# Optimization experiments

Hardware: AMD Instinct MI355X
Metric: run time of the kernel (lower is better)

## Reference

```python
import jax, jax.numpy as jnp
import numpy as np

B, S, D, H = 4, 2048, 1024, 16


def setup_inputs() -> dict:
    key = jax.random.key(0)
    ks = jax.random.split(key, 6)
    scale = 0.02
    return {
        "x": jax.random.normal(ks[0], (B, S, D), dtype=jnp.float32),
        "Wq": jax.random.normal(ks[1], (D, D), dtype=jnp.float32) * scale,
        "bq": jnp.zeros((D,), dtype=jnp.float32),
        "Wk": jax.random.normal(ks[2], (D, D), dtype=jnp.float32) * scale,
        "Wv": jax.random.normal(ks[3], (D, D), dtype=jnp.float32) * scale,
        "bv": jnp.zeros((D,), dtype=jnp.float32),
        "Wc": jax.random.normal(ks[4], (D, D), dtype=jnp.float32) * scale,
        "bc": jnp.zeros((D,), dtype=jnp.float32),
        "n_head": H,
    }


def reference(x, Wq, bq, Wk, Wv, bv, Wc, bc, n_head):
    # Projections (Conv1D == linear; k_proj has no bias since key_bias=False)
    q = x @ Wq + bq                      # [B, S, d_attn]
    k = x @ Wk                           # [B, S, d_attn]
    v = x @ Wv + bv                      # [B, S, d_attn]

    b, s, d_attn = q.shape
    d_head = d_attn // n_head
    # split heads -> [B, H, S, d_head]
    qh = q.reshape(b, s, n_head, d_head).transpose(0, 2, 1, 3)
    kh = k.reshape(b, s, n_head, d_head).transpose(0, 2, 1, 3)
    vh = v.reshape(b, s, n_head, d_head).transpose(0, 2, 1, 3)

    # scale applied to both q and k: 1/sqrt(sqrt(d_head))
    softmax_scale = 1.0 / np.sqrt(np.sqrt(d_head))
    qh = qh * softmax_scale
    kh = kh * softmax_scale

    w = jnp.einsum("bhqd,bhkd->bhqk", qh, kh)
    wtype = w.dtype
    w = w.astype(jnp.float32)
    n_q, n_k = w.shape[-2], w.shape[-1]
    # tril mask with diagonal offset n_k - n_q (supports incremental decode)
    mask = jnp.tril(jnp.ones((n_q, n_k), dtype=jnp.float32), k=n_k - n_q)[None, None]
    NEG = -1000000000.0
    w = w * mask + NEG * (1.0 - mask)
    w = jax.nn.softmax(w, axis=-1).astype(wtype)
    # attn_dropout rate 0 -> identity

    a = jnp.einsum("bhqk,bhkd->bhqd", w, vh)
    a = a.transpose(0, 2, 1, 3).reshape(b, s, d_attn)  # merge heads
    a = a @ Wc + bc
    # resid_dropout rate 0 -> identity
    hidden_state = jnp.stack([k, v])  # [2, B, S, d_attn]
    return (a, hidden_state)
```

## Files before the change

kernel.cpp:

```cpp
#include <hip/hip_runtime.h>
#include <stdint.h>

#define B_ 4
#define S_ 2048
#define D_ 1024
#define H_ 16
#define DH_ 64
#define MROWS (B_*S_)

typedef unsigned short ushortT;
typedef __attribute__((ext_vector_type(8))) short bf16x8;
typedef __attribute__((ext_vector_type(4))) float f32x4;

#define FLAG_BF16 1u
#define FLAG_F32  2u

__device__ __forceinline__ float b2f(ushortT u) {
  union { unsigned int i; float f; } v; v.i = ((unsigned int)u) << 16; return v.f;
}
__device__ __forceinline__ ushortT f2b(float f) {
  union { float f; unsigned int i; } v; v.f = f;
  unsigned int r = v.i + 0x7fffu + ((v.i >> 16) & 1u);
  return (ushortT)(r >> 16);
}

__device__ __forceinline__ float loadf(const ushortT* p) { return b2f(*p); }
__device__ __forceinline__ float loadf(const float* p)   { return *p; }
__device__ __forceinline__ unsigned int tob(ushortT u) { return u; }
__device__ __forceinline__ unsigned int tob(float f)   { return f2b(f); }

__device__ __forceinline__ void load8b(const ushortT* p, ushortT* u) {
  *(uint4*)u = *(const uint4*)p;
}
__device__ __forceinline__ void load8b(const float* p, ushortT* u) {
  float4 a = ((const float4*)p)[0], b = ((const float4*)p)[1];
  u[0] = f2b(a.x); u[1] = f2b(a.y); u[2] = f2b(a.z); u[3] = f2b(a.w);
  u[4] = f2b(b.x); u[5] = f2b(b.y); u[6] = f2b(b.z); u[7] = f2b(b.w);
}
template <typename T>
__device__ __forceinline__ void load16b(const T* p, ushortT* u) {
  load8b(p, u); load8b(p + 8, u + 8);
}

__device__ __forceinline__ void storef(ushortT* p, float v) { *p = f2b(v); }
__device__ __forceinline__ void storef(float* p, float v)   { *p = v; }

__device__ __forceinline__ void gload16(const ushortT* g, ushortT* l) {
  __builtin_amdgcn_global_load_lds(
      (const __attribute__((address_space(1))) void*)g,
      (__attribute__((address_space(3))) void*)l, 16, 0, 0);
}

__global__ void detect_dtype(const unsigned int* __restrict__ xw,
                             unsigned int* __restrict__ flag) {
  int lane = threadIdx.x;
  int cnt = 0;
  for (int i = lane; i < 2048; i += 64) {
    unsigned int e = (xw[i] >> 7) & 0xFFu;
    cnt += (e >= 0x68u && e <= 0x8Au) ? 1 : 0;
  }
#pragma unroll
  for (int off = 32; off; off >>= 1) cnt += __shfl_down(cnt, off);
  if (lane == 0) *flag = (cnt > 1024) ? FLAG_BF16 : FLAG_F32;
}

__global__ __launch_bounds__(256) void cvt_x_f32(
    const float* __restrict__ x, ushortT* __restrict__ xb,
    const unsigned int* __restrict__ flag) {
  if (*flag != FLAG_F32) return;
  const int total = MROWS * D_ / 8;
  for (int i = blockIdx.x * 256 + threadIdx.x; i < total; i += gridDim.x * 256) {
    float4 a = ((const float4*)x)[2 * i], b = ((const float4*)x)[2 * i + 1];
    ushortT u[8];
    u[0] = f2b(a.x); u[1] = f2b(a.y); u[2] = f2b(a.z); u[3] = f2b(a.w);
    u[4] = f2b(b.x); u[5] = f2b(b.y); u[6] = f2b(b.z); u[7] = f2b(b.w);
    ((uint4*)xb)[i] = *(uint4*)u;
  }
}

#define BK 32
#define BSTRIDE 40
#define GEMM_LDS (128 * BK + 128 * BSTRIDE)

template <typename TB, typename TOUT>
__device__ __forceinline__ void gemm_body(
    const ushortT* __restrict__ A, const TB* __restrict__ Bm,
    const TB* __restrict__ bias, TOUT* __restrict__ C, ushortT* smem)
{
  const int K = 1024, N = 1024;
  ushortT* As = smem;
  ushortT* Bs = smem + 128 * BK;
  int m0 = blockIdx.x * 128;
  int n0 = blockIdx.y * 128;
  int t = threadIdx.x;
  int lane = t & 63;
  int w = t >> 6;
  int wm = w >> 1, wn = w & 1;

  f32x4 acc[4][4] = {};

  const ushortT* a_src0 = A + (size_t)(m0 + (t >> 2)) * K + (t & 3) * 8;
  const ushortT* a_src1 = a_src0 + (size_t)64 * K;
  ushortT* a_dst0 = &As[(16 * w) * BK];
  ushortT* a_dst1 = &As[(64 + 16 * w) * BK];

  int cB = t & 127, r0 = (t >> 7) * 16;
  const TB* Bp0 = Bm + (size_t)r0 * N + n0 + cB;

  TB breg[16];
#pragma unroll
  for (int j = 0; j < 16; ++j) breg[j] = Bp0[(size_t)j * N];

  for (int kt = 0; kt < K; kt += BK) {
    gload16(a_src0 + kt, a_dst0);
    gload16(a_src1 + kt, a_dst1);
    {
      unsigned int* bd = (unsigned int*)&Bs[cB * BSTRIDE + r0];
#pragma unroll
      for (int j = 0; j < 8; ++j) {
        unsigned int lo = tob(breg[2 * j]);
        unsigned int hi = tob(breg[2 * j + 1]);
        bd[j] = lo | (hi << 16);
      }
    }
    __syncthreads();

    if (kt + BK < K) {
      const TB* bp = Bp0 + (size_t)(kt + BK) * N;
#pragma unroll
      for (int j = 0; j < 16; ++j) breg[j] = bp[(size_t)j * N];
    }

    int kq = (lane >> 4) * 8;
    int lm = lane & 15;
    bf16x8 af[4], bf[4];
#pragma unroll
    for (int mi = 0; mi < 4; ++mi)
      af[mi] = *(const bf16x8*)&As[(wm * 64 + mi * 16 + lm) * BK + kq];
#pragma unroll
    for (int ni = 0; ni < 4; ++ni)
      bf[ni] = *(const bf16x8*)&Bs[(wn * 64 + ni * 16 + lm) * BSTRIDE + kq];
#pragma unroll
    for (int mi = 0; mi < 4; ++mi)
#pragma unroll
      for (int ni = 0; ni < 4; ++ni)
        acc[mi][ni] = __builtin_amdgcn_mfma_f32_16x16x32_bf16(af[mi], bf[ni], acc[mi][ni], 0, 0, 0);
    __syncthreads();
  }

#pragma unroll
  for (int ni = 0; ni < 4; ++ni) {
    int col = n0 + wn * 64 + ni * 16 + (lane & 15);
    float bvv = bias ? loadf(bias + col) : 0.f;
#pragma unroll
    for (int mi = 0; mi < 4; ++mi) {
      int rbase = m0 + wm * 64 + mi * 16 + ((lane >> 4) * 4);
#pragma unroll
      for (int r = 0; r < 4; ++r)
        storef(C + (size_t)(rbase + r) * N + col, acc[mi][ni][r] + bvv);
    }
  }
}

#define KSTR 72
#define ATTN_LDS (2 * 64 * KSTR + 8 * 16 * KSTR)

template <typename TKV>
__device__ __forceinline__ void attn_body(
    const ushortT* __restrict__ Q, const TKV* __restrict__ Kh,
    const TKV* __restrict__ Vh, ushortT* __restrict__ O, ushortT* smem,
    int x, int h, int b)
{
  ushortT* Ks = smem;
  ushortT* Vs = smem + 64 * KSTR;
  ushortT* Ps = smem + 2 * 64 * KSTR;

  const int t = threadIdx.x, w = t >> 6, lane = t & 63;
  const int l15 = lane & 15, quad = lane >> 4;

  bf16x8 onesf;
  {
    ushortT u[8];
#pragma unroll
    for (int j = 0; j < 8; ++j) u[j] = 0x3F80;
    onesf = *(bf16x8*)u;
  }

  const TKV* kb = Kh + (size_t)(b * S_) * D_ + h * DH_;
  const TKV* vb = Vh + (size_t)(b * S_) * D_ + h * DH_;
  ushortT* Pw = Ps + w * (16 * KSTR);

  const int krow = t >> 3, kc = t & 7;
  const int vk = lane;

  for (int pi = 0; pi < 2; ++pi) {
    const int qt = pi ? (15 - x) : x;
    const int q0 = qt * 128;

    bf16x8 qf[2];
    {
      const ushortT* qp = Q + ((size_t)(b * S_) + q0 + w * 16 + l15) * D_ + h * DH_ + quad * 8;
#pragma unroll
      for (int c = 0; c < 2; ++c) {
        ushortT u[8];
        load8b(qp + c * 32, u);
        qf[c] = *(bf16x8*)u;
      }
    }

    f32x4 oac[4];
#pragma unroll
    for (int ni = 0; ni < 4; ++ni) oac[ni] = (f32x4){0.f, 0.f, 0.f, 0.f};
    f32x4 lac = (f32x4){0.f, 0.f, 0.f, 0.f};

    ushortT kr[8], vr[8];
    const int t0max = q0 + 64;

    {
      const TKV* kp = kb + (size_t)krow * D_ + kc * 8;
      load8b(kp, kr);
      const TKV* vp = vb + (size_t)vk * D_ + w * 8;
      load8b(vp, vr);
    }

    for (int t0 = 0; t0 <= t0max; t0 += 64) {
      *(uint4*)&Ks[krow * KSTR + kc * 8] = *(uint4*)kr;
#pragma unroll
      for (int j = 0; j < 8; ++j) Vs[(w * 8 + j) * KSTR + vk] = vr[j];
      __syncthreads();

      if (t0 + 64 <= t0max) {
        const TKV* kp = kb + (size_t)(t0 + 64 + krow) * D_ + kc * 8;
        load8b(kp, kr);
        const TKV* vp = vb + (size_t)(t0 + 64 + vk) * D_ + w * 8;
        load8b(vp, vr);
      }

      f32x4 sac[4];
#pragma unroll
      for (int ni = 0; ni < 4; ++ni) sac[ni] = (f32x4){0.f, 0.f, 0.f, 0.f};
      __builtin_amdgcn_s_setprio(1);
#pragma unroll
      for (int c = 0; c < 2; ++c)
#pragma unroll
        for (int ni = 0; ni < 4; ++ni) {
          bf16x8 bk = *(const bf16x8*)&Ks[(16 * ni + l15) * KSTR + c * 32 + quad * 8];
          sac[ni] = __builtin_amdgcn_mfma_f32_16x16x32_bf16(qf[c], bk, sac[ni], 0, 0, 0);
        }
      __builtin_amdgcn_s_setprio(0);

      if (t0 >= q0) {
        int koff = t0 - q0;
        int rowloc = w * 16 + quad * 4;
#pragma unroll
        for (int ni = 0; ni < 4; ++ni) {
          int kcol = koff + 16 * ni + l15;
#pragma unroll
          for (int r = 0; r < 4; ++r)
            if (kcol > rowloc + r) sac[ni][r] = -1e30f;
        }
      }

#pragma unroll
      for (int ni = 0; ni < 4; ++ni)
#pragma unroll
        for (int r = 0; r < 4; ++r) {
          float p = __expf(sac[ni][r] * 0.125f);
          Pw[(quad * 4 + r) * KSTR + 16 * ni + l15] = f2b(p);
        }

      __builtin_amdgcn_s_setprio(1);
#pragma unroll
      for (int c = 0; c < 2; ++c) {
        bf16x8 pa = *(const bf16x8*)&Pw[l15 * KSTR + c * 32 + quad * 8];
        lac = __builtin_amdgcn_mfma_f32_16x16x32_bf16(pa, onesf, lac, 0, 0, 0);
#pragma unroll
        for (int ni = 0; ni < 4; ++ni) {
          bf16x8 bv = *(const bf16x8*)&Vs[(16 * ni + l15) * KSTR + c * 32 + quad * 8];
          oac[ni] = __builtin_amdgcn_mfma_f32_16x16x32_bf16(pa, bv, oac[ni], 0, 0, 0);
        }
      }
      __builtin_amdgcn_s_setprio(0);
      __syncthreads();
    }

#pragma unroll
    for (int r = 0; r < 4; ++r) {
      float inv = 1.f / lac[r];
      ushortT* op = O + ((size_t)(b * S_) + q0 + w * 16 + quad * 4 + r) * D_ + h * DH_;
#pragma unroll
      for (int ni = 0; ni < 4; ++ni)
        op[16 * ni + l15] = f2b(oac[ni][r] * inv);
    }
  }
}

__global__ __launch_bounds__(256) void qkv_any(
    const void* x, const void* Wq, const void* Wk, const void* Wv,
    const void* bq, const void* bv, void* outp, const unsigned int* flag) {
  __shared__ __align__(16) ushortT smem[GEMM_LDS];
  int z = blockIdx.z;
  if (*flag == FLAG_BF16) {
    ushortT* o = (ushortT*)outp;
    ushortT* q = o;
    ushortT* k = o + (size_t)8388608;
    ushortT* v = o + (size_t)16777216;
    if (z == 0)      gemm_body<ushortT, ushortT>((const ushortT*)x, (const ushortT*)Wq, (const ushortT*)bq, q, smem);
    else if (z == 1) gemm_body<ushortT, ushortT>((const ushortT*)x, (const ushortT*)Wk, nullptr, k, smem);
    else             gemm_body<ushortT, ushortT>((const ushortT*)x, (const ushortT*)Wv, (const ushortT*)bv, v, smem);
  } else {
    float* of = (float*)outp;
    const ushortT* xb = (const ushortT*)outp;
    ushortT* q = (ushortT*)outp + (size_t)8388608;
    float* k = of + (size_t)8388608;
    float* v = of + (size_t)16777216;
    if (z == 0)      gemm_body<float, ushortT>(xb, (const float*)Wq, (const float*)bq, q, smem);
    else if (z == 1) gemm_body<float, float>(xb, (const float*)Wk, nullptr, k, smem);
    else             gemm_body<float, float>(xb, (const float*)Wv, (const float*)bv, v, smem);
  }
}

__global__ __launch_bounds__(512, 2) void attn_any(
    void* outp, ushortT* O, const unsigned int* flag) {
  __shared__ __align__(16) ushortT smem[ATTN_LDS];
  int bid = (int)blockIdx.x + 8 * (int)blockIdx.y + 128 * (int)blockIdx.z;
  int lid = (bid & 7) * 64 + (bid >> 3);
  int x = lid & 7, h = (lid >> 3) & 15, b = lid >> 7;
  if (*flag == FLAG_BF16) {
    ushortT* o = (ushortT*)outp;
    attn_body<ushortT>(o, o + (size_t)8388608, o + (size_t)16777216, O, smem, x, h, b);
  } else {
    const ushortT* q = (const ushortT*)outp + (size_t)8388608;
    const float* of = (const float*)outp;
    attn_body<float>(q, of + (size_t)8388608, of + (size_t)16777216, O, smem, x, h, b);
  }
}

__global__ __launch_bounds__(256) void proj_any(
    const ushortT* A, const void* Wc, const void* bc, void* outp,
    const unsigned int* flag) {
  __shared__ __align__(16) ushortT smem[GEMM_LDS];
  if (*flag == FLAG_BF16)
    gemm_body<ushortT, ushortT>(A, (const ushortT*)Wc, (const ushortT*)bc, (ushortT*)outp, smem);
  else
    gemm_body<float, float>(A, (const float*)Wc, (const float*)bc, (float*)outp, smem);
}

extern "C" void kernel_launch(void* const* d_in, const int* in_sizes, int n_in,
                              void* d_out, int out_size, void* d_ws, size_t ws_size,
                              hipStream_t stream) {
  (void)in_sizes; (void)n_in; (void)out_size; (void)ws_size;

  unsigned int* flagp = (unsigned int*)d_ws;
  ushortT* attn_ws = (ushortT*)((char*)d_ws + 256);

  detect_dtype<<<1, 64, 0, stream>>>((const unsigned int*)d_in[0], flagp);
  cvt_x_f32<<<2048, 256, 0, stream>>>((const float*)d_in[0], (ushortT*)d_out, flagp);

  dim3 gq(MROWS / 128, D_ / 128, 3);
  dim3 gp(MROWS / 128, D_ / 128);
  dim3 ga(S_ / 256, H_, B_);

  qkv_any<<<gq, 256, 0, stream>>>(d_in[0], d_in[1], d_in[3], d_in[4],
                                  d_in[2], d_in[5], d_out, flagp);
  attn_any<<<ga, 512, 0, stream>>>(d_out, attn_ws, flagp);
  proj_any<<<gp, 256, 0, stream>>>(attn_ws, d_in[6], d_in[7], d_out, flagp);
}
```

Baseline: 382.8 us.

## Pre-transpose weights to bf16 and use direct-to-LDS B^T GEMM

```diff
diff --git a/kernel.cpp b/kernel.cpp
--- a/kernel.cpp
+++ b/kernel.cpp
@@ -75,6 +75,100 @@
     u[0] = f2b(a.x); u[1] = f2b(a.y); u[2] = f2b(a.z); u[3] = f2b(a.w);
     u[4] = f2b(b.x); u[5] = f2b(b.y); u[6] = f2b(b.z); u[7] = f2b(b.w);
     ((uint4*)xb)[i] = *(uint4*)u;
+  }
+}
+
+__global__ __launch_bounds__(256) void transpose_w(
+    const void* W0, const void* W1, const void* W2, const void* W3,
+    ushortT* dst0, ushortT* dstc, const unsigned int* flag) {
+  __shared__ ushortT tile[64][72];
+  int z = blockIdx.z;
+  const void* W = (z == 0) ? W0 : (z == 1) ? W1 : (z == 2) ? W2 : W3;
+  ushortT* dst = (z < 3) ? dst0 + (size_t)z * 1048576 : dstc;
+  int n0 = blockIdx.x * 64, k0 = blockIdx.y * 64;
+  int t = threadIdx.x;
+  bool isb = (*flag == FLAG_BF16);
+  for (int s = t; s < 512; s += 256) {
+    int kr = s >> 3, nc = (s & 7) * 8;
+    ushortT u[8];
+    if (isb) load8b((const ushortT*)W + (size_t)(k0 + kr) * D_ + n0 + nc, u);
+    else     load8b((const float*)W   + (size_t)(k0 + kr) * D_ + n0 + nc, u);
+#pragma unroll
+    for (int j = 0; j < 8; ++j) tile[kr][nc + j] = u[j];
+  }
+  __syncthreads();
+  for (int s = t; s < 512; s += 256) {
+    int nr = s >> 3, kc = (s & 7) * 8;
+    ushortT u[8];
+#pragma unroll
+    for (int j = 0; j < 8; ++j) u[j] = tile[kc + j][nr];
+    *(uint4*)(dst + (size_t)(n0 + nr) * D_ + k0 + kc) = *(uint4*)u;
+  }
+}
+
+#define GEMM_BT_LDS (2 * 128 * 32)
+
+template <typename TBIAS, typename TOUT>
+__device__ __forceinline__ void gemm_bt(
+    const ushortT* __restrict__ A, const ushortT* __restrict__ Bt,
+    const TBIAS* __restrict__ bias, TOUT* __restrict__ C, ushortT* smem)
+{
+  const int K = 1024, N = 1024;
+  ushortT* As = smem;
+  ushortT* Bs = smem + 128 * 32;
+  int m0 = blockIdx.x * 128;
+  int n0 = blockIdx.y * 128;
+  int t = threadIdx.x;
+  int lane = t & 63;
+  int w = t >> 6;
+  int wm = w >> 1, wn = w & 1;
+
+  f32x4 acc[4][4] = {};
+
+  const ushortT* a_src0 = A  + (size_t)(m0 + (t >> 2)) * K + (t & 3) * 8;
+  const ushortT* a_src1 = a_src0 + (size_t)64 * K;
+  const ushortT* b_src0 = Bt + (size_t)(n0 + (t >> 2)) * K + (t & 3) * 8;
+  const ushortT* b_src1 = b_src0 + (size_t)64 * K;
+  ushortT* a_dst0 = &As[(16 * w) * 32];
+  ushortT* a_dst1 = &As[(64 + 16 * w) * 32];
+  ushortT* b_dst0 = &Bs[(16 * w) * 32];
+  ushortT* b_dst1 = &Bs[(64 + 16 * w) * 32];
+
+  for (int kt = 0; kt < K; kt += 32) {
+    gload16(a_src0 + kt, a_dst0);
+    gload16(a_src1 + kt, a_dst1);
+    gload16(b_src0 + kt, b_dst0);
+    gload16(b_src1 + kt, b_dst1);
+    __syncthreads();
+
+    int kq = (lane >> 4) * 8;
+    int lm = lane & 15;
+    bf16x8 af[4], bf[4];
+#pragma unroll
+    for (int mi = 0; mi < 4; ++mi)
+      af[mi] = *(const bf16x8*)&As[(wm * 64 + mi * 16 + lm) * 32 + kq];
+#pragma unroll
+    for (int ni = 0; ni < 4; ++ni)
+      bf[ni] = *(const bf16x8*)&Bs[(wn * 64 + ni * 16 + lm) * 32 + kq];
+#pragma unroll
+    for (int mi = 0; mi < 4; ++mi)
+#pragma unroll
+      for (int ni = 0; ni < 4; ++ni)
+        acc[mi][ni] = __builtin_amdgcn_mfma_f32_16x16x32_bf16(af[mi], bf[ni], acc[mi][ni], 0, 0, 0);
+    __syncthreads();
+  }
+
+#pragma unroll
+  for (int ni = 0; ni < 4; ++ni) {
+    int col = n0 + wn * 64 + ni * 16 + (lane & 15);
+    float bvv = bias ? loadf(bias + col) : 0.f;
+#pragma unroll
+    for (int mi = 0; mi < 4; ++mi) {
+      int rbase = m0 + wm * 64 + mi * 16 + ((lane >> 4) * 4);
+#pragma unroll
+      for (int r = 0; r < 4; ++r)
+        storef(C + (size_t)(rbase + r) * N + col, acc[mi][ni][r] + bvv);
+    }
   }
 }
 
@@ -296,27 +390,24 @@
 }
 
 __global__ __launch_bounds__(256) void qkv_any(
-    const void* x, const void* Wq, const void* Wk, const void* Wv,
-    const void* bq, const void* bv, void* outp, const unsigned int* flag) {
-  __shared__ __align__(16) ushortT smem[GEMM_LDS];
+    const void* x, const ushortT* wt, const void* bq, const void* bv,
+    void* outp, const unsigned int* flag) {
+  __shared__ __align__(16) ushortT smem[GEMM_BT_LDS];
   int z = blockIdx.z;
+  const ushortT* Bt = wt + (size_t)z * 1048576;
   if (*flag == FLAG_BF16) {
     ushortT* o = (ushortT*)outp;
-    ushortT* q = o;
-    ushortT* k = o + (size_t)8388608;
-    ushortT* v = o + (size_t)16777216;
-    if (z == 0)      gemm_body<ushortT, ushortT>((const ushortT*)x, (const ushortT*)Wq, (const ushortT*)bq, q, smem);
-    else if (z == 1) gemm_body<ushortT, ushortT>((const ushortT*)x, (const ushortT*)Wk, nullptr, k, smem);
-    else             gemm_body<ushortT, ushortT>((const ushortT*)x, (const ushortT*)Wv, (const ushortT*)bv, v, smem);
+    const ushortT* A = (const ushortT*)x;
+    if (z == 0)      gemm_bt<ushortT, ushortT>(A, Bt, (const ushortT*)bq, o, smem);
+    else if (z == 1) gemm_bt<ushortT, ushortT>(A, Bt, nullptr, o + (size_t)8388608, smem);
+    else             gemm_bt<ushortT, ushortT>(A, Bt, (const ushortT*)bv, o + (size_t)16777216, smem);
   } else {
     float* of = (float*)outp;
-    const ushortT* xb = (const ushortT*)outp;
+    const ushortT* A = (const ushortT*)outp;
     ushortT* q = (ushortT*)outp + (size_t)8388608;
-    float* k = of + (size_t)8388608;
-    float* v = of + (size_t)16777216;
-    if (z == 0)      gemm_body<float, ushortT>(xb, (const float*)Wq, (const float*)bq, q, smem);
-    else if (z == 1) gemm_body<float, float>(xb, (const float*)Wk, nullptr, k, smem);
-    else             gemm_body<float, float>(xb, (const float*)Wv, (const float*)bv, v, smem);
+    if (z == 0)      gemm_bt<float, ushortT>(A, Bt, (const float*)bq, q, smem);
+    else if (z == 1) gemm_bt<float, float>(A, Bt, nullptr, of + (size_t)8388608, smem);
+    else             gemm_bt<float, float>(A, Bt, (const float*)bv, of + (size_t)16777216, smem);
   }
 }
 
@@ -336,7 +427,17 @@
   }
 }
 
-__global__ __launch_bounds__(256) void proj_any(
+__global__ __launch_bounds__(256) void proj_bt(
+    const ushortT* A, const ushortT* wct, const void* bc, void* outp,
+    const unsigned int* flag) {
+  __shared__ __align__(16) ushortT smem[GEMM_BT_LDS];
+  if (*flag == FLAG_BF16)
+    gemm_bt<ushortT, ushortT>(A, wct, (const ushortT*)bc, (ushortT*)outp, smem);
+  else
+    gemm_bt<float, float>(A, wct, (const float*)bc, (float*)outp, smem);
+}
+
+__global__ __launch_bounds__(256) void proj_legacy(
     const ushortT* A, const void* Wc, const void* bc, void* outp,
     const unsigned int* flag) {
   __shared__ __align__(16) ushortT smem[GEMM_LDS];
@@ -349,20 +450,28 @@
 extern "C" void kernel_launch(void* const* d_in, const int* in_sizes, int n_in,
                               void* d_out, int out_size, void* d_ws, size_t ws_size,
                               hipStream_t stream) {
-  (void)in_sizes; (void)n_in; (void)out_size; (void)ws_size;
+  (void)in_sizes; (void)n_in; (void)out_size;
 
   unsigned int* flagp = (unsigned int*)d_ws;
   ushortT* attn_ws = (ushortT*)((char*)d_ws + 256);
+  ushortT* wct_p = (ushortT*)((char*)d_ws + 256 + 16777216);
+  bool wct_ok = ws_size >= (size_t)(256 + 16777216 + 2097152);
 
   detect_dtype<<<1, 64, 0, stream>>>((const unsigned int*)d_in[0], flagp);
   cvt_x_f32<<<2048, 256, 0, stream>>>((const float*)d_in[0], (ushortT*)d_out, flagp);
+
+  dim3 gt(D_ / 64, D_ / 64, wct_ok ? 4 : 3);
+  transpose_w<<<gt, 256, 0, stream>>>(d_in[1], d_in[3], d_in[4], d_in[6],
+                                      attn_ws, wct_p, flagp);
 
   dim3 gq(MROWS / 128, D_ / 128, 3);
   dim3 gp(MROWS / 128, D_ / 128);
   dim3 ga(S_ / 256, H_, B_);
 
-  qkv_any<<<gq, 256, 0, stream>>>(d_in[0], d_in[1], d_in[3], d_in[4],
-                                  d_in[2], d_in[5], d_out, flagp);
+  qkv_any<<<gq, 256, 0, stream>>>(d_in[0], attn_ws, d_in[2], d_in[5], d_out, flagp);
   attn_any<<<ga, 512, 0, stream>>>(d_out, attn_ws, flagp);
-  proj_any<<<gp, 256, 0, stream>>>(attn_ws, d_in[6], d_in[7], d_out, flagp);
-}
+  if (wct_ok)
+    proj_bt<<<gp, 256, 0, stream>>>(attn_ws, wct_p, d_in[7], d_out, flagp);
+  else
+    proj_legacy<<<gp, 256, 0, stream>>>(attn_ws, d_in[6], d_in[7], d_out, flagp);
+}
```

Result: faster. 334.4 us (-12.6%).
